# Kernel tuning notes

Measured on AMD Instinct MI355X. Metric: run time of the kernel, lower is better.

Reference implementation:

```python
import jax, jax.numpy as jnp
import numpy as np

VOCAB = 90000
MAX_ID = 95000
EFFECT_DIM = 758
ADD_DIM = 10
EMBED_DIM = 768  # EFFECT_DIM + ADD_DIM
CTX = 1024
MAX_SYN = 8


def setup_inputs() -> dict:
    key = jax.random.key(0)
    k_ids, k_emb, k_rev, k_tab, k_msk = jax.random.split(key, 5)
    ids = jax.random.randint(k_ids, (CTX,), 0, VOCAB, dtype=jnp.int64)
    W_emb = jax.random.normal(k_emb, (MAX_ID, EFFECT_DIM), dtype=jnp.float32)
    W_rev = jax.random.normal(k_rev, (EMBED_DIM, MAX_ID), dtype=jnp.float32)
    padding = 0.1 * jnp.ones((CTX, ADD_DIM), dtype=jnp.float32)
    # synonym ids live in [VOCAB, MAX_ID); only some slots are active (variable-length lists)
    syn_table = jax.random.randint(k_tab, (MAX_ID, MAX_SYN), VOCAB, MAX_ID, dtype=jnp.int32)
    syn_mask = jax.random.randint(k_msk, (MAX_ID, MAX_SYN), 0, 2, dtype=jnp.int32)
    # tokens >= VOCAB (synonym ids themselves) have no synonyms
    syn_mask = syn_mask.at[VOCAB:].set(0)
    return {"ids": ids, "W_emb": W_emb, "W_rev": W_rev, "padding": padding,
            "syn_table": syn_table, "syn_mask": syn_mask}


def reference(ids, W_emb, W_rev, padding, syn_table, syn_mask):
    # VirtualEmbedding: base gather + masked synonym gather/scale/accumulate.
    # i_sum is computed BEFORE the synonym loop in the original, so each
    # synonym contribution is independent -> vectorized masked reduction.
    # (Dropout in eval mode is the identity.)
    base = W_emb[ids]                              # [L, D]
    syn_ids = syn_table[ids]                       # [L, K]
    syn = W_emb[syn_ids]                           # [L, K, D]
    mask = syn_mask[ids].astype(base.dtype)        # [L, K]
    i_sum = jnp.sum(base, axis=-1, keepdims=True)  # [L, 1]
    s_sum = jnp.sum(syn, axis=-1)                  # [L, K]
    d = i_sum / s_sum                              # [L, K]
    emb = base + jnp.einsum('lk,lkd->ld', mask * d, syn)
    # concat fixed context padding, then ReverseEmbedding projection to vocab
    full = jnp.concatenate([emb, padding], axis=1)  # [L, EMBED_DIM]
    return full @ W_rev                             # [L, MAX_ID]
```

## Files before the change

### kernel.cpp

```cpp
#include <hip/hip_runtime.h>
#include <stdint.h>

#define EFFECT_DIM 758
#define ADD_DIM 10
#define EMBED_DIM 768
#define NCOLS 95000
#define NSYN 8
#define NROWS 1024
#define NTILE_N 743

typedef __attribute__((ext_vector_type(8))) __bf16 bf16x8;
typedef __attribute__((ext_vector_type(16))) float f32x16;
typedef __attribute__((ext_vector_type(4))) uint32_t u32x4;

static __device__ __forceinline__ uint32_t pack2(float a, float b) {
  uint32_t r;
  asm("v_cvt_pk_bf16_f32 %0, %1, %2" : "=v"(r) : "v"(a), "v"(b));
  return r;
}

#define GLOAD16(src, dst)                                                   \
  __builtin_amdgcn_global_load_lds(                                         \
      (const __attribute__((address_space(1))) uint32_t*)(src),             \
      (__attribute__((address_space(3))) uint32_t*)(dst), 16, 0, 0)

#define F4C(f, i) ((i) == 0 ? (f).x : (i) == 1 ? (f).y : (i) == 2 ? (f).z : (f).w)

__global__ __launch_bounds__(256) void emb_kernel(
    const int* __restrict__ ids, const float* __restrict__ W_emb,
    const float* __restrict__ padding, const int* __restrict__ syn_table,
    const int* __restrict__ syn_mask, char* __restrict__ ws)
{
  const int l = blockIdx.x;
  const int t = threadIdx.x;
  const int id = ids[l];
  int sid[NSYN];
  int msk[NSYN];
#pragma unroll
  for (int k = 0; k < NSYN; ++k) {
    sid[k] = syn_table[id * NSYN + k];
    msk[k] = syn_mask[id * NSYN + k];
  }

  double p[9] = {0, 0, 0, 0, 0, 0, 0, 0, 0};
  for (int d = t; d < EFFECT_DIM; d += 256) {
    p[0] += (double)W_emb[(size_t)id * EFFECT_DIM + d];
#pragma unroll
    for (int k = 0; k < NSYN; ++k)
      p[k + 1] += (double)W_emb[(size_t)sid[k] * EFFECT_DIM + d];
  }

  __shared__ double s_red[9][4];
  const int w = t >> 6;
#pragma unroll
  for (int k = 0; k < 9; ++k) {
    double v = p[k];
#pragma unroll
    for (int off = 32; off > 0; off >>= 1) v += __shfl_down(v, off, 64);
    if ((t & 63) == 0) s_red[k][w] = v;
  }
  __syncthreads();

  const double isum = s_red[0][0] + s_red[0][1] + s_red[0][2] + s_red[0][3];
  float coef[NSYN];
#pragma unroll
  for (int k = 0; k < NSYN; ++k) {
    double ss = s_red[k + 1][0] + s_red[k + 1][1] + s_red[k + 1][2] + s_red[k + 1][3];
    coef[k] = msk[k] ? (float)(isum / ss) : 0.0f;
  }

  const int mt = l >> 7;
  const int r  = l & 127;
  const int sw = (r & 7) << 4;
  char* wbase = ws + (size_t)mt * (12 * 16384);

  for (int j = t; j < 384; j += 256) {
    const int d0 = 2 * j;
    float v0, v1;
    if (d0 < EFFECT_DIM) {
      const float* bp = W_emb + (size_t)id * EFFECT_DIM + d0;
      v0 = bp[0];
      v1 = bp[1];
#pragma unroll
      for (int k = 0; k < NSYN; ++k) {
        const float* sp = W_emb + (size_t)sid[k] * EFFECT_DIM + d0;
        v0 = fmaf(coef[k], sp[0], v0);
        v1 = fmaf(coef[k], sp[1], v1);
      }
    } else {
      v0 = padding[l * ADD_DIM + (d0 - EFFECT_DIM)];
      v1 = padding[l * ADD_DIM + (d0 + 1 - EFFECT_DIM)];
    }
    const int ks = j >> 5;
    const int jl = j & 31;
    *(uint32_t*)(wbase + ks * 16384 + r * 128 + ((jl * 4) ^ sw)) = pack2(v0, v1);
  }
}

__global__ __launch_bounds__(256) void conv_kernel(
    const float* __restrict__ Wrev, char* __restrict__ Bbuf)
{
  __shared__ char lds[16384];
  const int t   = threadIdx.x;
  const int nt  = blockIdx.x;
  const int ks  = blockIdx.y;
  const int nl4 = t & 31;
  const int kc  = t >> 5;
  const int gn4 = nt * 128 + nl4 * 4;
  const bool valid = (gn4 + 4) <= NCOLS;

  float4 v[8];
  const float* p = Wrev + (size_t)(ks * 64 + kc * 8) * NCOLS + gn4;
#pragma unroll
  for (int j = 0; j < 8; ++j)
    v[j] = valid ? *(const float4*)(p + (size_t)j * NCOLS)
                 : float4{0.0f, 0.0f, 0.0f, 0.0f};

#pragma unroll
  for (int i = 0; i < 4; ++i) {
    const int n = nl4 * 4 + i;
    u32x4 u;
#pragma unroll
    for (int j2 = 0; j2 < 4; ++j2)
      u[j2] = pack2(F4C(v[2 * j2], i), F4C(v[2 * j2 + 1], i));
    *(u32x4*)(lds + n * 128 + ((kc * 16) ^ ((n & 7) << 4))) = u;
  }
  __syncthreads();

  char* dst = Bbuf + (size_t)(nt * 12 + ks) * 16384;
#pragma unroll
  for (int i = 0; i < 4; ++i)
    *(u32x4*)(dst + t * 16 + i * 4096) = *(const u32x4*)(lds + t * 16 + i * 4096);
}

__global__ __launch_bounds__(256, 4) void gemm_pre(
    const char* __restrict__ Abuf, const char* __restrict__ Bbuf,
    float* __restrict__ out)
{
  __shared__ char lds[32768];
  const int t  = threadIdx.x;
  const int l  = t & 63;
  const int w  = t >> 6;
  const int wm = w >> 1;
  const int wn = w & 1;
  const int lr = l & 31;
  const int lh = l >> 5;

  const int wgid = blockIdx.x;
  const int xcd  = wgid & 7;
  const int work = xcd * 743 + (wgid >> 3);
  const int mt = work & 7;
  const int nt = work >> 3;
  const int n0 = nt * 128;

  f32x16 acc[2][2] = {};

  const char* asrc = Abuf + (size_t)mt * (12 * 16384);
  const char* bsrc = Bbuf + (size_t)nt * (12 * 16384);

  for (int ks = 0; ks < 12; ++ks) {
    {
      const char* sa = asrc + ks * 16384 + w * 1024 + l * 16;
      const char* sb = bsrc + ks * 16384 + w * 1024 + l * 16;
      char* da = lds + w * 1024;
      char* db = lds + 16384 + w * 1024;
#pragma unroll
      for (int i = 0; i < 4; ++i) {
        GLOAD16(sa + i * 4096, da + i * 4096);
        GLOAD16(sb + i * 4096, db + i * 4096);
      }
    }
    __syncthreads();

    bf16x8 af[2][4], bg[2][4];
#pragma unroll
    for (int mr = 0; mr < 2; ++mr) {
      const int rr = wm * 64 + mr * 32 + lr;
      const int swz = (rr & 7) << 4;
#pragma unroll
      for (int kk = 0; kk < 4; ++kk) {
        const int c2 = kk * 32 + lh * 16;
        af[mr][kk] = *(const bf16x8*)(lds + rr * 128 + (c2 ^ swz));
      }
    }
#pragma unroll
    for (int nr = 0; nr < 2; ++nr) {
      const int rr = wn * 64 + nr * 32 + lr;
      const int swz = (rr & 7) << 4;
#pragma unroll
      for (int kk = 0; kk < 4; ++kk) {
        const int c2 = kk * 32 + lh * 16;
        bg[nr][kk] = *(const bf16x8*)(lds + 16384 + rr * 128 + (c2 ^ swz));
      }
    }
#pragma unroll
    for (int kk = 0; kk < 4; ++kk)
#pragma unroll
      for (int mr = 0; mr < 2; ++mr)
#pragma unroll
        for (int nr = 0; nr < 2; ++nr)
          acc[mr][nr] = __builtin_amdgcn_mfma_f32_32x32x16_bf16(
              af[mr][kk], bg[nr][kk], acc[mr][nr], 0, 0, 0);
    __syncthreads();
  }

#pragma unroll
  for (int mr = 0; mr < 2; ++mr)
#pragma unroll
    for (int nr = 0; nr < 2; ++nr) {
      const int gc = n0 + wn * 64 + nr * 32 + lr;
      if (gc < NCOLS) {
#pragma unroll
        for (int reg = 0; reg < 16; ++reg) {
          const int row = (reg & 3) + 8 * (reg >> 2) + 4 * lh;
          const int gr = mt * 128 + wm * 64 + mr * 32 + row;
          out[(size_t)gr * NCOLS + gc] = acc[mr][nr][reg];
        }
      }
    }
}

__global__ __launch_bounds__(256, 2) void gemm_kernel(
    const float* __restrict__ Wrev, const char* __restrict__ Abuf,
    float* __restrict__ out)
{
  __shared__ char lds[32768];
  const int t  = threadIdx.x;
  const int l  = t & 63;
  const int w  = t >> 6;
  const int wm = w >> 1;
  const int wn = w & 1;
  const int lr = l & 31;
  const int lh = l >> 5;
  const int mt = blockIdx.x;
  const int n0 = blockIdx.y * 128;

  f32x16 acc[2][2] = {};

  const char* asrc = Abuf + (size_t)mt * (12 * 16384);
  const int nl = t & 127;
  const int kc_base = t >> 7;
  const int gn = n0 + nl;
  const int bswz = (nl & 7) << 4;

  for (int ks = 0; ks < 12; ++ks) {
    {
      const char* s = asrc + ks * 16384 + w * 1024 + l * 16;
      char* d = lds + w * 1024;
#pragma unroll
      for (int i = 0; i < 4; ++i)
        GLOAD16(s + i * 4096, d + i * 4096);
    }
#pragma unroll
    for (int task = 0; task < 4; ++task) {
      const int kc = kc_base + task * 2;
      float v[8];
      const float* p = Wrev + (size_t)(ks * 64 + kc * 8) * NCOLS + gn;
#pragma unroll
      for (int j = 0; j < 8; ++j)
        v[j] = (gn < NCOLS) ? p[(size_t)j * NCOLS] : 0.0f;
      u32x4 u;
#pragma unroll
      for (int j = 0; j < 4; ++j)
        u[j] = pack2(v[2 * j], v[2 * j + 1]);
      *(u32x4*)(lds + 16384 + nl * 128 + ((kc * 16) ^ bswz)) = u;
    }
    __syncthreads();

    bf16x8 af[2][4], bg[2][4];
#pragma unroll
    for (int mr = 0; mr < 2; ++mr) {
      const int rr = wm * 64 + mr * 32 + lr;
      const int swz = (rr & 7) << 4;
#pragma unroll
      for (int kk = 0; kk < 4; ++kk) {
        const int c2 = kk * 32 + lh * 16;
        af[mr][kk] = *(const bf16x8*)(lds + rr * 128 + (c2 ^ swz));
      }
    }
#pragma unroll
    for (int nr = 0; nr < 2; ++nr) {
      const int rr = wn * 64 + nr * 32 + lr;
      const int swz = (rr & 7) << 4;
#pragma unroll
      for (int kk = 0; kk < 4; ++kk) {
        const int c2 = kk * 32 + lh * 16;
        bg[nr][kk] = *(const bf16x8*)(lds + 16384 + rr * 128 + (c2 ^ swz));
      }
    }
#pragma unroll
    for (int kk = 0; kk < 4; ++kk)
#pragma unroll
      for (int mr = 0; mr < 2; ++mr)
#pragma unroll
        for (int nr = 0; nr < 2; ++nr)
          acc[mr][nr] = __builtin_amdgcn_mfma_f32_32x32x16_bf16(
              af[mr][kk], bg[nr][kk], acc[mr][nr], 0, 0, 0);
    __syncthreads();
  }

#pragma unroll
  for (int mr = 0; mr < 2; ++mr)
#pragma unroll
    for (int nr = 0; nr < 2; ++nr) {
      const int gc = n0 + wn * 64 + nr * 32 + lr;
      if (gc < NCOLS) {
#pragma unroll
        for (int reg = 0; reg < 16; ++reg) {
          const int row = (reg & 3) + 8 * (reg >> 2) + 4 * lh;
          const int gr = mt * 128 + wm * 64 + mr * 32 + row;
          out[(size_t)gr * NCOLS + gc] = acc[mr][nr][reg];
        }
      }
    }
}

extern "C" void kernel_launch(void* const* d_in, const int* in_sizes, int n_in,
                              void* d_out, int out_size, void* d_ws, size_t ws_size,
                              hipStream_t stream) {
  const int*   ids       = (const int*)d_in[0];
  const float* W_emb     = (const float*)d_in[1];
  const float* W_rev     = (const float*)d_in[2];
  const float* padding   = (const float*)d_in[3];
  const int*   syn_table = (const int*)d_in[4];
  const int*   syn_mask  = (const int*)d_in[5];
  float* out = (float*)d_out;
  char*  ws  = (char*)d_ws;

  const size_t A_BYTES = (size_t)8 * 12 * 16384;
  const size_t B_BYTES = (size_t)NTILE_N * 12 * 16384;

  hipLaunchKernelGGL(emb_kernel, dim3(NROWS), dim3(256), 0, stream,
                     ids, W_emb, padding, syn_table, syn_mask, ws);

  if (ws_size >= A_BYTES + B_BYTES) {
    char* Bbuf = ws + A_BYTES;
    hipLaunchKernelGGL(conv_kernel, dim3(NTILE_N, 12), dim3(256), 0, stream,
                       W_rev, Bbuf);
    hipLaunchKernelGGL(gemm_pre, dim3(8 * NTILE_N), dim3(256), 0, stream,
                       ws, Bbuf, out);
  } else {
    hipLaunchKernelGGL(gemm_kernel, dim3(8, NTILE_N), dim3(256), 0, stream,
                       W_rev, ws, out);
  }
}
```

Baseline: 356.8 us.

## Double-buffer LDS in gemm_pre with 512 threads and prefetched K stages

Reworks the precomputed-B GEMM kernel to use 8 waves (512 threads) per block, each computing a 64x32 sub-tile instead of 64x64. It double-buffers the LDS A/B tiles (64 KiB total) and issues the next K-slice's global-to-LDS loads before computing the current one, using explicit vmcnt waits, sched barriers and s_setprio around the MFMAs. The aim is to overlap global memory latency with matrix math and raise wave-level parallelism. In exchange, LDS per block doubles, which may limit how many blocks fit on a CU, and each wave now does fewer MFMAs per LDS load.

```diff
diff --git a/kernel.cpp b/kernel.cpp
--- a/kernel.cpp
+++ b/kernel.cpp
@@ -133,16 +133,16 @@
     *(u32x4*)(dst + t * 16 + i * 4096) = *(const u32x4*)(lds + t * 16 + i * 4096);
 }
 
-__global__ __launch_bounds__(256, 4) void gemm_pre(
+__global__ __launch_bounds__(512, 4) void gemm_pre(
     const char* __restrict__ Abuf, const char* __restrict__ Bbuf,
     float* __restrict__ out)
 {
-  __shared__ char lds[32768];
+  __shared__ char lds[65536];
   const int t  = threadIdx.x;
   const int l  = t & 63;
   const int w  = t >> 6;
-  const int wm = w >> 1;
-  const int wn = w & 1;
+  const int wm = w >> 2;
+  const int wn = w & 3;
   const int lr = l & 31;
   const int lh = l >> 5;
 
@@ -153,71 +153,71 @@
   const int nt = work >> 3;
   const int n0 = nt * 128;
 
-  f32x16 acc[2][2] = {};
+  f32x16 acc[2] = {};
 
   const char* asrc = Abuf + (size_t)mt * (12 * 16384);
   const char* bsrc = Bbuf + (size_t)nt * (12 * 16384);
+  const int soff = w * 2048 + l * 16;
+
+#define STAGE(buf, ksi)                                                      \
+  {                                                                          \
+    const char* sa = asrc + (ksi)*16384 + soff;                              \
+    const char* sb = bsrc + (ksi)*16384 + soff;                              \
+    char* da = lds + (buf)*32768 + w * 2048;                                 \
+    char* db = lds + (buf)*32768 + 16384 + w * 2048;                         \
+    GLOAD16(sa, da);                                                         \
+    GLOAD16(sa + 1024, da + 1024);                                           \
+    GLOAD16(sb, db);                                                         \
+    GLOAD16(sb + 1024, db + 1024);                                           \
+  }
+
+  STAGE(0, 0);
+
+  const int ra0 = wm * 64 + lr, ra1 = ra0 + 32;
+  const int rb  = wn * 32 + lr;
+  const int sa0 = (ra0 & 7) << 4, sa1 = (ra1 & 7) << 4;
+  const int sbz = (rb & 7) << 4;
 
   for (int ks = 0; ks < 12; ++ks) {
-    {
-      const char* sa = asrc + ks * 16384 + w * 1024 + l * 16;
-      const char* sb = bsrc + ks * 16384 + w * 1024 + l * 16;
-      char* da = lds + w * 1024;
-      char* db = lds + 16384 + w * 1024;
-#pragma unroll
-      for (int i = 0; i < 4; ++i) {
-        GLOAD16(sa + i * 4096, da + i * 4096);
-        GLOAD16(sb + i * 4096, db + i * 4096);
-      }
-    }
-    __syncthreads();
-
-    bf16x8 af[2][4], bg[2][4];
-#pragma unroll
-    for (int mr = 0; mr < 2; ++mr) {
-      const int rr = wm * 64 + mr * 32 + lr;
-      const int swz = (rr & 7) << 4;
-#pragma unroll
-      for (int kk = 0; kk < 4; ++kk) {
-        const int c2 = kk * 32 + lh * 16;
-        af[mr][kk] = *(const bf16x8*)(lds + rr * 128 + (c2 ^ swz));
-      }
-    }
-#pragma unroll
-    for (int nr = 0; nr < 2; ++nr) {
-      const int rr = wn * 64 + nr * 32 + lr;
-      const int swz = (rr & 7) << 4;
-#pragma unroll
-      for (int kk = 0; kk < 4; ++kk) {
-        const int c2 = kk * 32 + lh * 16;
-        bg[nr][kk] = *(const bf16x8*)(lds + 16384 + rr * 128 + (c2 ^ swz));
-      }
-    }
-#pragma unroll
-    for (int kk = 0; kk < 4; ++kk)
-#pragma unroll
-      for (int mr = 0; mr < 2; ++mr)
-#pragma unroll
-        for (int nr = 0; nr < 2; ++nr)
-          acc[mr][nr] = __builtin_amdgcn_mfma_f32_32x32x16_bf16(
-              af[mr][kk], bg[nr][kk], acc[mr][nr], 0, 0, 0);
-    __syncthreads();
-  }
-
-#pragma unroll
-  for (int mr = 0; mr < 2; ++mr)
-#pragma unroll
-    for (int nr = 0; nr < 2; ++nr) {
-      const int gc = n0 + wn * 64 + nr * 32 + lr;
-      if (gc < NCOLS) {
-#pragma unroll
-        for (int reg = 0; reg < 16; ++reg) {
-          const int row = (reg & 3) + 8 * (reg >> 2) + 4 * lh;
-          const int gr = mt * 128 + wm * 64 + mr * 32 + row;
-          out[(size_t)gr * NCOLS + gc] = acc[mr][nr][reg];
-        }
-      }
-    }
+    if (ks < 11) {
+      STAGE((ks + 1) & 1, ks + 1);
+      __builtin_amdgcn_sched_barrier(0);
+      asm volatile("s_waitcnt vmcnt(4)");
+    } else {
+      __builtin_amdgcn_sched_barrier(0);
+      asm volatile("s_waitcnt vmcnt(0)");
+    }
+    __builtin_amdgcn_sched_barrier(0);
+    __builtin_amdgcn_s_barrier();
+
+    const char* base = lds + (ks & 1) * 32768;
+#pragma unroll
+    for (int kk = 0; kk < 4; ++kk) {
+      const int c2 = kk * 32 + lh * 16;
+      bf16x8 a0 = *(const bf16x8*)(base + ra0 * 128 + (c2 ^ sa0));
+      bf16x8 a1 = *(const bf16x8*)(base + ra1 * 128 + (c2 ^ sa1));
+      bf16x8 b0 = *(const bf16x8*)(base + 16384 + rb * 128 + (c2 ^ sbz));
+      __builtin_amdgcn_s_setprio(1);
+      acc[0] = __builtin_amdgcn_mfma_f32_32x32x16_bf16(a0, b0, acc[0], 0, 0, 0);
+      acc[1] = __builtin_amdgcn_mfma_f32_32x32x16_bf16(a1, b0, acc[1], 0, 0, 0);
+      __builtin_amdgcn_s_setprio(0);
+    }
+    __builtin_amdgcn_sched_barrier(0);
+    __builtin_amdgcn_s_barrier();
+  }
+#undef STAGE
+
+  const int gc = n0 + wn * 32 + lr;
+  if (gc < NCOLS) {
+#pragma unroll
+    for (int mr = 0; mr < 2; ++mr)
+#pragma unroll
+      for (int reg = 0; reg < 16; ++reg) {
+        const int row = (reg & 3) + 8 * (reg >> 2) + 4 * lh;
+        const int gr = mt * 128 + wm * 64 + mr * 32 + row;
+        out[(size_t)gr * NCOLS + gc] = acc[mr][reg];
+      }
+  }
 }
 
 __global__ __launch_bounds__(256, 2) void gemm_kernel(
@@ -337,7 +337,7 @@
     char* Bbuf = ws + A_BYTES;
     hipLaunchKernelGGL(conv_kernel, dim3(NTILE_N, 12), dim3(256), 0, stream,
                        W_rev, Bbuf);
-    hipLaunchKernelGGL(gemm_pre, dim3(8 * NTILE_N), dim3(256), 0, stream,
+    hipLaunchKernelGGL(gemm_pre, dim3(8 * NTILE_N), dim3(512), 0, stream,
                        ws, Bbuf, out);
   } else {
     hipLaunchKernelGGL(gemm_kernel, dim3(8, NTILE_N), dim3(256), 0, stream,
```

After: 359.1 us. No clear change (+0.7%).
